# Kernel tuning notes

Hardware: AMD Instinct MI355X
Metric: run time of the kernel (lower is better)

## Reference

```python
import jax, jax.numpy as jnp
import numpy as np

N_NODES = 50000
N_EDGES = 800000
IN_DIM = 128
HID = 32
HEADS = 4
OUT_DIM = 128
NEG_SLOPE = 0.2


def setup_inputs() -> dict:
    key = jax.random.key(0)
    ks = jax.random.split(key, 10)
    s = lambda fan_in: 1.0 / np.sqrt(fan_in)
    return {
        "x": jax.random.normal(ks[0], (N_NODES, IN_DIM), dtype=jnp.float32),
        "edge_index": jax.random.randint(ks[1], (2, N_EDGES), 0, N_NODES, dtype=jnp.int64),
        # encoder GATConv: in=IN_DIM, out=HID, heads=HEADS (concat)
        "W1": jax.random.normal(ks[2], (IN_DIM, HEADS * HID), dtype=jnp.float32) * s(IN_DIM),
        "att_src1": jax.random.normal(ks[3], (HEADS, HID), dtype=jnp.float32) * s(HID),
        "att_dst1": jax.random.normal(ks[4], (HEADS, HID), dtype=jnp.float32) * s(HID),
        "b1": jnp.zeros((HEADS * HID,), dtype=jnp.float32),
        # decoder GATConv: in=HEADS*HID, out=OUT_DIM, heads=1
        "W2": jax.random.normal(ks[5], (HEADS * HID, OUT_DIM), dtype=jnp.float32) * s(HEADS * HID),
        "att_src2": jax.random.normal(ks[6], (1, OUT_DIM), dtype=jnp.float32) * s(OUT_DIM),
        "att_dst2": jax.random.normal(ks[7], (1, OUT_DIM), dtype=jnp.float32) * s(OUT_DIM),
        "b2": jnp.zeros((OUT_DIM,), dtype=jnp.float32),
    }


def _gat_conv(x, src, dst, W, att_src, att_dst, bias, heads, out_ch):
    """PyG-style GATConv (v1), eval mode (dropout off), self-loops already in src/dst."""
    n = x.shape[0]
    h = (x @ W).reshape(n, heads, out_ch)                 # [N,H,C]
    a_src = jnp.einsum("nhc,hc->nh", h, att_src)          # [N,H]
    a_dst = jnp.einsum("nhc,hc->nh", h, att_dst)          # [N,H]
    e = jax.nn.leaky_relu(a_src[src] + a_dst[dst], NEG_SLOPE)  # [E,H]
    # segment softmax over destination neighborhoods
    e_max = jax.ops.segment_max(e, dst, num_segments=n)   # [N,H]
    e_exp = jnp.exp(e - e_max[dst])
    denom = jax.ops.segment_sum(e_exp, dst, num_segments=n)
    alpha = e_exp / (denom[dst] + 1e-16)                  # [E,H]
    msg = h[src] * alpha[:, :, None]                      # [E,H,C]
    out = jax.ops.segment_sum(msg, dst, num_segments=n)   # [N,H,C]
    return out.reshape(n, heads * out_ch) + bias


def reference(x, edge_index, W1, att_src1, att_dst1, b1, W2, att_src2, att_dst2, b2):
    n = x.shape[0]
    loops = jnp.arange(n, dtype=edge_index.dtype)
    src = jnp.concatenate([edge_index[0], loops])
    dst = jnp.concatenate([edge_index[1], loops])
    z = jax.nn.relu(_gat_conv(x, src, dst, W1, att_src1, att_dst1, b1, HEADS, HID))
    x_hat = jax.nn.relu(_gat_conv(z, src, dst, W2, att_src2, att_dst2, b2, 1, OUT_DIM))
    return x_hat
```

## Files before the change

### kernel.cpp

```cpp
#include <hip/hip_runtime.h>
#include <hip/hip_bf16.h>
#include <cstddef>

#define N_NODES 50000
#define N_EDGES_RAW 800000
#define E_TOT (N_EDGES_RAW + N_NODES)
#define DIM 128
#define NEG_SLOPE 0.2f

#define NBUCK 196
#define CHUNK 4096
#define NBLK_E ((E_TOT + CHUNK - 1) / CHUNK)
#define CONV_BLKS 3125
#define GB 782

typedef __attribute__((ext_vector_type(8))) short bf16x8;
typedef __attribute__((ext_vector_type(4))) float f32x4;

__device__ __forceinline__ ushort f2bf(float f) {
  unsigned u = __float_as_uint(f);
  return (ushort)((u + 0x7FFFu + ((u >> 16) & 1u)) >> 16);
}
__device__ __forceinline__ float bf2f_lo(uint u) {
  return __uint_as_float(u << 16);
}
__device__ __forceinline__ float bf2f_hi(uint u) {
  return __uint_as_float(u & 0xFFFF0000u);
}

__device__ __forceinline__ void get_edge(const int* __restrict__ ei, int is64,
                                         int e, int& s, int& d) {
  if (e >= N_EDGES_RAW) { s = e - N_EDGES_RAW; d = s; return; }
  if (is64) {
    s = ei[2 * (size_t)e];
    d = ei[2 * ((size_t)N_EDGES_RAW + (size_t)e)];
  } else {
    s = ei[e];
    d = ei[N_EDGES_RAW + e];
  }
}

__device__ __forceinline__ int detect_inline(const int* __restrict__ ei,
                                             int* sflag) {
  const int t = threadIdx.x;
  if (t < 64) {
    int hi = ei[2 * t + 1];
    unsigned long long b = __ballot(hi != 0);
    if (t == 0) *sflag = (b == 0ULL) ? 1 : 0;
  }
  __syncthreads();
  return *sflag;
}

__device__ __forceinline__ void prep_one(const float* __restrict__ w,
                                         const float* __restrict__ atts,
                                         const float* __restrict__ attd,
                                         ushort* __restrict__ wtx,
                                         int H, int idx) {
  const int c = idx >> 7, k = idx & 127;
  const int C = 128 / H;
  float v;
  if (c < 128) {
    v = w[k * 128 + c];
  } else if (c < 128 + H) {
    const int hd = c - 128;
    float s = 0.f;
    for (int j = 0; j < C; ++j) s += w[k * 128 + hd * C + j] * atts[hd * C + j];
    v = s;
  } else if (c < 128 + 2 * H) {
    const int hd = c - 128 - H;
    float s = 0.f;
    for (int j = 0; j < C; ++j) s += w[k * 128 + hd * C + j] * attd[hd * C + j];
    v = s;
  } else {
    v = 0.f;
  }
  wtx[idx] = f2bf(v);
}

__global__ __launch_bounds__(256) void mega_setup(
    const float* __restrict__ W1, const float* __restrict__ as1,
    const float* __restrict__ ad1, ushort* __restrict__ wtx1,
    const float* __restrict__ W2, const float* __restrict__ as2,
    const float* __restrict__ ad2, ushort* __restrict__ wtx2,
    const float* __restrict__ x, ushort* __restrict__ x_bf,
    const int* __restrict__ ei, int* __restrict__ hist_mat,
    unsigned* __restrict__ pairs) {
  const int b = blockIdx.x, t = threadIdx.x;
  if (b < 72) {
    prep_one(W1, as1, ad1, wtx1, 4, b * 256 + t);
  } else if (b < 144) {
    prep_one(W2, as2, ad2, wtx2, 1, (b - 72) * 256 + t);
  } else if (b < 144 + CONV_BLKS) {
    const int base = (b - 144) * 2048 + t * 8;
    float4 v0 = *(const float4*)(x + base);
    float4 v1 = *(const float4*)(x + base + 4);
    ushort u[8];
    u[0] = f2bf(v0.x); u[1] = f2bf(v0.y); u[2] = f2bf(v0.z); u[3] = f2bf(v0.w);
    u[4] = f2bf(v1.x); u[5] = f2bf(v1.y); u[6] = f2bf(v1.z); u[7] = f2bf(v1.w);
    *(uint4*)(x_bf + base) = *(const uint4*)u;
  } else {
    __shared__ int hist[NBUCK];
    __shared__ int sflag;
    const int cb = b - 144 - CONV_BLKS;
    if (t < NBUCK) hist[t] = 0;
    const int is64 = detect_inline(ei, &sflag);
    __syncthreads();
    const int e0 = cb * CHUNK;
#pragma unroll
    for (int i = 0; i < CHUNK / 256; ++i) {
      int e = e0 + i * 256 + t;
      if (e < E_TOT) {
        int s, d;
        get_edge(ei, is64, e, s, d);
        pairs[e] = (unsigned)s | ((unsigned)d << 16);
        atomicAdd(&hist[d >> 8], 1);
      }
    }
    __syncthreads();
    if (t < NBUCK) hist_mat[cb * NBUCK + t] = hist[t];
  }
}

__global__ __launch_bounds__(256) void bucket_scatter(
    const unsigned* __restrict__ pairs, const int* __restrict__ hist_mat,
    unsigned* __restrict__ tmp, int* __restrict__ bstart_g) {
  __shared__ int wtot[4];
  __shared__ int sbase[NBUCK];
  __shared__ int shist[NBUCK];
  const int b = blockIdx.x, t = threadIdx.x, lane = t & 63, wid = t >> 6;
  int tot = 0, pre = 0;
  if (t < NBUCK) {
    for (int bb = 0; bb < NBLK_E; ++bb) {
      int v = hist_mat[bb * NBUCK + t];
      pre += (bb < b) ? v : 0;
      tot += v;
    }
    shist[t] = 0;
  }
  int sc = tot;
#pragma unroll
  for (int m = 1; m < 64; m <<= 1) {
    int o = __shfl_up(sc, m, 64);
    if (lane >= m) sc += o;
  }
  if (lane == 63) wtot[wid] = sc;
  __syncthreads();
  int off = 0;
  for (int w = 0; w < wid; ++w) off += wtot[w];
  const int excl = off + sc - tot;
  if (t < NBUCK) sbase[t] = excl + pre;
  if (b == 0) {
    if (t < NBUCK) bstart_g[t] = excl;
    if (t == 255) bstart_g[NBUCK] = off + sc;
  }
  __syncthreads();
  const int e0 = b * CHUNK;
  unsigned pr_[CHUNK / 256];
  int rk[CHUNK / 256];
#pragma unroll
  for (int i = 0; i < CHUNK / 256; ++i) {
    int e = e0 + i * 256 + t;
    if (e < E_TOT) {
      unsigned pr = pairs[e];
      pr_[i] = pr;
      rk[i] = atomicAdd(&shist[pr >> 24], 1);
    }
  }
#pragma unroll
  for (int i = 0; i < CHUNK / 256; ++i) {
    int e = e0 + i * 256 + t;
    if (e < E_TOT) tmp[sbase[pr_[i] >> 24] + rk[i]] = pr_[i];
  }
}

__device__ __forceinline__ void bucket_sort_body(int b,
                                                 const unsigned* __restrict__ tmp,
                                                 const int* __restrict__ bstart,
                                                 int* __restrict__ csr_src,
                                                 int* __restrict__ rp,
                                                 int* __restrict__ deg) {
  __shared__ int cnt[256];
  __shared__ int cur[256];
  __shared__ int wtot2[4];
  const int t = threadIdx.x, lane = t & 63, wid = t >> 6;
  const int p0 = bstart[b], p1 = bstart[b + 1];
  cnt[t] = 0;
  __syncthreads();
  for (int j = p0 + t; j < p1; j += 256) {
    unsigned pr = tmp[j];
    atomicAdd(&cnt[(pr >> 16) & 255u], 1);
  }
  __syncthreads();
  int v = cnt[t];
  int sc = v;
#pragma unroll
  for (int m = 1; m < 64; m <<= 1) {
    int o = __shfl_up(sc, m, 64);
    if (lane >= m) sc += o;
  }
  if (lane == 63) wtot2[wid] = sc;
  __syncthreads();
  int off = 0;
  for (int w = 0; w < wid; ++w) off += wtot2[w];
  const int excl = off + sc - v;
  const int node = b * 256 + t;
  if (node < N_NODES) {
    deg[node] = v;
    rp[node] = p0 + excl;
  }
  cur[t] = excl;
  __syncthreads();
  for (int j = p0 + t; j < p1; j += 256) {
    unsigned pr = tmp[j];
    int ld = (int)((pr >> 16) & 255u);
    int r = atomicAdd(&cur[ld], 1);
    csr_src[p0 + r] = (int)(pr & 0xFFFFu);
  }
}

template <int H>
__device__ __forceinline__ void gemm_att_body(int blk,
                                              const ushort* __restrict__ in_bf,
                                              const ushort* __restrict__ wtx,
                                              ushort* __restrict__ h_bf,
                                              float* __restrict__ a_src,
                                              float* __restrict__ a_dst) {
  const int wid = threadIdx.x >> 6;
  const int lane = threadIdx.x & 63;
  const int tile = blk * 4 + wid;
  if (tile >= N_NODES / 16) return;
  const int row0 = tile * 16;
  const int rA = lane & 15;
  const int g = lane >> 4;

  f32x4 acc[9];
#pragma unroll
  for (int ct = 0; ct < 9; ++ct) acc[ct] = (f32x4){0.f, 0.f, 0.f, 0.f};

#pragma unroll
  for (int ks = 0; ks < 4; ++ks) {
    const int k0 = ks * 32 + g * 8;
    bf16x8 af = *(const bf16x8*)(in_bf + (size_t)(row0 + rA) * DIM + k0);
#pragma unroll
    for (int ct = 0; ct < 9; ++ct) {
      bf16x8 bf = *(const bf16x8*)(wtx + (size_t)(ct * 16 + rA) * 128 + k0);
      acc[ct] = __builtin_amdgcn_mfma_f32_16x16x32_bf16(af, bf, acc[ct], 0, 0, 0);
    }
  }

#pragma unroll
  for (int ct = 0; ct < 8; ++ct) {
#pragma unroll
    for (int r = 0; r < 4; ++r) {
      const int row = row0 + g * 4 + r;
      h_bf[(size_t)row * DIM + ct * 16 + rA] = f2bf(acc[ct][r]);
    }
  }
  if (rA < 2 * H) {
#pragma unroll
    for (int r = 0; r < 4; ++r) {
      const int row = row0 + g * 4 + r;
      if (rA < H)
        a_src[(size_t)row * H + rA] = acc[8][r];
      else
        a_dst[(size_t)row * H + (rA - H)] = acc[8][r];
    }
  }
}

__global__ __launch_bounds__(256) void gemm4_sort(
    const ushort* __restrict__ x_bf, const ushort* __restrict__ wtx1,
    ushort* __restrict__ h_bf, float* __restrict__ a_src,
    float* __restrict__ a_dst, const unsigned* __restrict__ tmp,
    const int* __restrict__ bstart, int* __restrict__ csr_src,
    int* __restrict__ rp, int* __restrict__ deg) {
  if (blockIdx.x < GB)
    gemm_att_body<4>(blockIdx.x, x_bf, wtx1, h_bf, a_src, a_dst);
  else
    bucket_sort_body(blockIdx.x - GB, tmp, bstart, csr_src, rp, deg);
}

__global__ __launch_bounds__(256) void gemm_att1(const ushort* __restrict__ in_bf,
                                                 const ushort* __restrict__ wtx,
                                                 ushort* __restrict__ h_bf,
                                                 float* __restrict__ a_src,
                                                 float* __restrict__ a_dst) {
  gemm_att_body<1>(blockIdx.x, in_bf, wtx, h_bf, a_src, a_dst);
}

template <int H, bool OBF>
__global__ __launch_bounds__(256) void node_agg(const int* __restrict__ rp,
                                                const int* __restrict__ deg,
                                                const int* __restrict__ csr_src,
                                                const ushort* __restrict__ h_bf,
                                                const float* __restrict__ a_src,
                                                const float* __restrict__ a_dst,
                                                const float* __restrict__ bias,
                                                void* __restrict__ outp) {
  __shared__ float p_lds[4][H][64];
  __shared__ int s_lds[4][64];
  const int wid = threadIdx.x >> 6;
  const int lane = threadIdx.x & 63;
  const int node = blockIdx.x * 4 + wid;
  if (node >= N_NODES) return;
  const int head = (H == 4) ? (lane >> 4) : 0;
  const int beg = rp[node];
  const int dg = deg[node];
  const int* __restrict__ srcs = csr_src + beg;

  float ad[H];
#pragma unroll
  for (int h = 0; h < H; ++h) ad[h] = a_dst[(size_t)node * H + h];

  float sden[H];
#pragma unroll
  for (int h = 0; h < H; ++h) sden[h] = 0.f;
  float ax = 0.f, ay = 0.f;

  for (int c0 = 0; c0 < dg; c0 += 64) {
    const int cnt = min(64, dg - c0);
    if (lane < cnt) {
      int s = srcs[c0 + lane];
      s_lds[wid][lane] = s;
      if (H == 4) {
        float4 as4 = ((const float4*)a_src)[s];
        float vv[4] = {as4.x, as4.y, as4.z, as4.w};
#pragma unroll
        for (int h = 0; h < 4; ++h) {
          float v = vv[h] + ad[h];
          v = v > 0.f ? v : NEG_SLOPE * v;
          v = fminf(fmaxf(v, -60.f), 80.f);
          float p = __expf(v);
          sden[h] += p;
          p_lds[wid][h][lane] = p;
        }
      } else {
        float v = a_src[s] + ad[0];
        v = v > 0.f ? v : NEG_SLOPE * v;
        v = fminf(fmaxf(v, -60.f), 80.f);
        float p = __expf(v);
        sden[0] += p;
        p_lds[wid][0][lane] = p;
      }
    }
    int j = 0;
    for (; j + 8 <= cnt; j += 8) {
#pragma unroll
      for (int u = 0; u < 8; ++u) {
        int s = s_lds[wid][j + u];
        float p = p_lds[wid][head][j + u];
        uint hv = *(const uint*)(h_bf + (size_t)s * DIM + 2 * lane);
        ax += p * bf2f_lo(hv);
        ay += p * bf2f_hi(hv);
      }
    }
    for (; j < cnt; ++j) {
      int s = s_lds[wid][j];
      float p = p_lds[wid][head][j];
      uint hv = *(const uint*)(h_bf + (size_t)s * DIM + 2 * lane);
      ax += p * bf2f_lo(hv);
      ay += p * bf2f_hi(hv);
    }
  }

#pragma unroll
  for (int h = 0; h < H; ++h) {
#pragma unroll
    for (int m = 1; m < 64; m <<= 1) sden[h] += __shfl_xor(sden[h], m);
  }
  const float inv = 1.f / sden[head];

  float2 bv = ((const float2*)bias)[lane];
  float ox = fmaxf(ax * inv + bv.x, 0.f);
  float oy = fmaxf(ay * inv + bv.y, 0.f);
  if (OBF) {
    uint u = (uint)f2bf(ox) | ((uint)f2bf(oy) << 16);
    ((uint*)((ushort*)outp + (size_t)node * DIM))[lane] = u;
  } else {
    ((float2*)((float*)outp + (size_t)node * DIM))[lane] = make_float2(ox, oy);
  }
}

extern "C" void kernel_launch(void* const* d_in, const int* in_sizes, int n_in,
                              void* d_out, int out_size, void* d_ws, size_t ws_size,
                              hipStream_t stream) {
  const float* x   = (const float*)d_in[0];
  const int*   ei  = (const int*)d_in[1];
  const float* W1  = (const float*)d_in[2];
  const float* as1 = (const float*)d_in[3];
  const float* ad1 = (const float*)d_in[4];
  const float* b1  = (const float*)d_in[5];
  const float* W2  = (const float*)d_in[6];
  const float* as2 = (const float*)d_in[7];
  const float* ad2 = (const float*)d_in[8];
  const float* b2  = (const float*)d_in[9];
  float* out = (float*)d_out;

  char* ws = (char*)d_ws;
  const size_t F_H = (size_t)N_NODES * DIM;
  ushort*   h_bf    = (ushort*)ws;
  ushort*   z_bf    = h_bf + F_H;
  ushort*   x_bf    = z_bf + F_H;
  float*    a_src   = (float*)(x_bf + F_H);
  float*    a_dst   = a_src + 200000;
  int*      deg     = (int*)(a_dst + 200000);
  int*      rp      = deg + N_NODES;
  int*      csr_src = rp + N_NODES;
  unsigned* tmp     = (unsigned*)(csr_src + E_TOT);
  unsigned* pairs   = tmp + E_TOT;
  int*      hist_mat= (int*)(pairs + E_TOT);
  int*      bstart  = hist_mat + NBLK_E * NBUCK;
  ushort*   wtx1    = (ushort*)(bstart + NBUCK + 3);
  ushort*   wtx2    = wtx1 + 144 * 128;

  const int MEGA = 144 + CONV_BLKS + NBLK_E;

  hipLaunchKernelGGL(mega_setup, dim3(MEGA), dim3(256), 0, stream,
                     W1, as1, ad1, wtx1, W2, as2, ad2, wtx2, x, x_bf, ei,
                     hist_mat, pairs);
  hipLaunchKernelGGL(bucket_scatter, dim3(NBLK_E), dim3(256), 0, stream,
                     pairs, hist_mat, tmp, bstart);
  hipLaunchKernelGGL(gemm4_sort, dim3(GB + NBUCK), dim3(256), 0, stream,
                     x_bf, wtx1, h_bf, a_src, a_dst, tmp, bstart, csr_src, rp, deg);
  hipLaunchKernelGGL((node_agg<4, true>), dim3((N_NODES + 3) / 4), dim3(256), 0,
                     stream, rp, deg, csr_src, h_bf, a_src, a_dst, b1, z_bf);

  hipLaunchKernelGGL(gemm_att1, dim3(GB), dim3(256), 0, stream,
                     z_bf, wtx2, h_bf, a_src, a_dst);
  hipLaunchKernelGGL((node_agg<1, false>), dim3((N_NODES + 3) / 4), dim3(256), 0,
                     stream, rp, deg, csr_src, h_bf, a_src, a_dst, b2, out);
}
```

Before: 165.6 us.

## Aggregate 16 nodes per block with block-cooperative edge score precompute

Each node-aggregation block now covers 16 consecutive nodes, and each wave handles 4 of them in turn. The block's contiguous CSR edge range is staged in 512-edge chunks, and all 256 threads compute the exp scores into LDS together, instead of each wave working only on its own node's few edges. To make this possible, the CSR array now stores the packed (dst, src) word, so the dst attention term can be looked up per edge. The softmax denominator is accumulated per lane in the gather loop, which removes the cross-lane shuffle reductions. The cost is block-level barriers, a quarter as many blocks, and serial per-node gathers within each wave.

```diff
diff --git a/kernel.cpp b/kernel.cpp
--- a/kernel.cpp
+++ b/kernel.cpp
@@ -13,6 +13,7 @@
 #define NBLK_E ((E_TOT + CHUNK - 1) / CHUNK)
 #define CONV_BLKS 3125
 #define GB 782
+#define ECHUNK 512
 
 typedef __attribute__((ext_vector_type(8))) short bf16x8;
 typedef __attribute__((ext_vector_type(4))) float f32x4;
@@ -177,7 +178,7 @@
 __device__ __forceinline__ void bucket_sort_body(int b,
                                                  const unsigned* __restrict__ tmp,
                                                  const int* __restrict__ bstart,
-                                                 int* __restrict__ csr_src,
+                                                 unsigned* __restrict__ csr2,
                                                  int* __restrict__ rp,
                                                  int* __restrict__ deg) {
   __shared__ int cnt[256];
@@ -215,7 +216,7 @@
     unsigned pr = tmp[j];
     int ld = (int)((pr >> 16) & 255u);
     int r = atomicAdd(&cur[ld], 1);
-    csr_src[p0 + r] = (int)(pr & 0xFFFFu);
+    csr2[p0 + r] = pr;
   }
 }
 
@@ -273,12 +274,12 @@
     const ushort* __restrict__ x_bf, const ushort* __restrict__ wtx1,
     ushort* __restrict__ h_bf, float* __restrict__ a_src,
     float* __restrict__ a_dst, const unsigned* __restrict__ tmp,
-    const int* __restrict__ bstart, int* __restrict__ csr_src,
+    const int* __restrict__ bstart, unsigned* __restrict__ csr2,
     int* __restrict__ rp, int* __restrict__ deg) {
   if (blockIdx.x < GB)
     gemm_att_body<4>(blockIdx.x, x_bf, wtx1, h_bf, a_src, a_dst);
   else
-    bucket_sort_body(blockIdx.x - GB, tmp, bstart, csr_src, rp, deg);
+    bucket_sort_body(blockIdx.x - GB, tmp, bstart, csr2, rp, deg);
 }
 
 __global__ __launch_bounds__(256) void gemm_att1(const ushort* __restrict__ in_bf,
@@ -292,93 +293,90 @@
 template <int H, bool OBF>
 __global__ __launch_bounds__(256) void node_agg(const int* __restrict__ rp,
                                                 const int* __restrict__ deg,
-                                                const int* __restrict__ csr_src,
+                                                const unsigned* __restrict__ csr2,
                                                 const ushort* __restrict__ h_bf,
                                                 const float* __restrict__ a_src,
                                                 const float* __restrict__ a_dst,
                                                 const float* __restrict__ bias,
                                                 void* __restrict__ outp) {
-  __shared__ float p_lds[4][H][64];
-  __shared__ int s_lds[4][64];
-  const int wid = threadIdx.x >> 6;
-  const int lane = threadIdx.x & 63;
-  const int node = blockIdx.x * 4 + wid;
-  if (node >= N_NODES) return;
+  __shared__ float p_lds[ECHUNK][H];
+  __shared__ int s_lds[ECHUNK];
+  const int t = threadIdx.x;
+  const int wid = t >> 6;
+  const int lane = t & 63;
+  const int nbase = blockIdx.x * 16;
   const int head = (H == 4) ? (lane >> 4) : 0;
-  const int beg = rp[node];
-  const int dg = deg[node];
-  const int* __restrict__ srcs = csr_src + beg;
-
-  float ad[H];
-#pragma unroll
-  for (int h = 0; h < H; ++h) ad[h] = a_dst[(size_t)node * H + h];
-
-  float sden[H];
-#pragma unroll
-  for (int h = 0; h < H; ++h) sden[h] = 0.f;
-  float ax = 0.f, ay = 0.f;
-
-  for (int c0 = 0; c0 < dg; c0 += 64) {
-    const int cnt = min(64, dg - c0);
-    if (lane < cnt) {
-      int s = srcs[c0 + lane];
-      s_lds[wid][lane] = s;
+
+  int rp_m[4], dg_m[4];
+#pragma unroll
+  for (int m = 0; m < 4; ++m) {
+    int n = nbase + 4 * wid + m;
+    rp_m[m] = rp[n];
+    dg_m[m] = deg[n];
+  }
+  const int blockbase = rp[nbase];
+  const int blockend = rp[nbase + 15] + deg[nbase + 15];
+
+  float ax[4], ay[4], sden[4];
+#pragma unroll
+  for (int m = 0; m < 4; ++m) { ax[m] = 0.f; ay[m] = 0.f; sden[m] = 0.f; }
+
+  for (int base = blockbase; base < blockend; base += ECHUNK) {
+    const int cnt = min(ECHUNK, blockend - base);
+    for (int k = t; k < cnt; k += 256) {
+      unsigned pr = csr2[base + k];
+      int s = (int)(pr & 0xFFFFu);
+      int d = (int)(pr >> 16);
+      s_lds[k] = s;
       if (H == 4) {
         float4 as4 = ((const float4*)a_src)[s];
-        float vv[4] = {as4.x, as4.y, as4.z, as4.w};
+        float4 ad4 = ((const float4*)a_dst)[d];
+        float vv[4] = {as4.x + ad4.x, as4.y + ad4.y, as4.z + ad4.z, as4.w + ad4.w};
 #pragma unroll
         for (int h = 0; h < 4; ++h) {
-          float v = vv[h] + ad[h];
+          float v = vv[h];
           v = v > 0.f ? v : NEG_SLOPE * v;
           v = fminf(fmaxf(v, -60.f), 80.f);
-          float p = __expf(v);
-          sden[h] += p;
-          p_lds[wid][h][lane] = p;
+          p_lds[k][h] = __expf(v);
         }
       } else {
-        float v = a_src[s] + ad[0];
+        float v = a_src[s] + a_dst[d];
         v = v > 0.f ? v : NEG_SLOPE * v;
         v = fminf(fmaxf(v, -60.f), 80.f);
-        float p = __expf(v);
-        sden[0] += p;
-        p_lds[wid][0][lane] = p;
+        p_lds[k][0] = __expf(v);
       }
     }
-    int j = 0;
-    for (; j + 8 <= cnt; j += 8) {
-#pragma unroll
-      for (int u = 0; u < 8; ++u) {
-        int s = s_lds[wid][j + u];
-        float p = p_lds[wid][head][j + u];
+    __syncthreads();
+#pragma unroll
+    for (int m = 0; m < 4; ++m) {
+      const int lo = max(rp_m[m], base) - base;
+      const int hi = min(rp_m[m] + dg_m[m], base + cnt) - base;
+#pragma unroll 2
+      for (int j = lo; j < hi; ++j) {
+        int s = s_lds[j];
+        float p = p_lds[j][head];
         uint hv = *(const uint*)(h_bf + (size_t)s * DIM + 2 * lane);
-        ax += p * bf2f_lo(hv);
-        ay += p * bf2f_hi(hv);
+        ax[m] += p * bf2f_lo(hv);
+        ay[m] += p * bf2f_hi(hv);
+        sden[m] += p;
       }
     }
-    for (; j < cnt; ++j) {
-      int s = s_lds[wid][j];
-      float p = p_lds[wid][head][j];
-      uint hv = *(const uint*)(h_bf + (size_t)s * DIM + 2 * lane);
-      ax += p * bf2f_lo(hv);
-      ay += p * bf2f_hi(hv);
-    }
-  }
-
-#pragma unroll
-  for (int h = 0; h < H; ++h) {
-#pragma unroll
-    for (int m = 1; m < 64; m <<= 1) sden[h] += __shfl_xor(sden[h], m);
-  }
-  const float inv = 1.f / sden[head];
-
-  float2 bv = ((const float2*)bias)[lane];
-  float ox = fmaxf(ax * inv + bv.x, 0.f);
-  float oy = fmaxf(ay * inv + bv.y, 0.f);
-  if (OBF) {
-    uint u = (uint)f2bf(ox) | ((uint)f2bf(oy) << 16);
-    ((uint*)((ushort*)outp + (size_t)node * DIM))[lane] = u;
-  } else {
-    ((float2*)((float*)outp + (size_t)node * DIM))[lane] = make_float2(ox, oy);
+    __syncthreads();
+  }
+
+  const float2 bv = ((const float2*)bias)[lane];
+#pragma unroll
+  for (int m = 0; m < 4; ++m) {
+    const int node = nbase + 4 * wid + m;
+    const float inv = 1.f / sden[m];
+    float ox = fmaxf(ax[m] * inv + bv.x, 0.f);
+    float oy = fmaxf(ay[m] * inv + bv.y, 0.f);
+    if (OBF) {
+      uint u = (uint)f2bf(ox) | ((uint)f2bf(oy) << 16);
+      ((uint*)((ushort*)outp + (size_t)node * DIM))[lane] = u;
+    } else {
+      ((float2*)((float*)outp + (size_t)node * DIM))[lane] = make_float2(ox, oy);
+    }
   }
 }
 
@@ -406,8 +404,8 @@
   float*    a_dst   = a_src + 200000;
   int*      deg     = (int*)(a_dst + 200000);
   int*      rp      = deg + N_NODES;
-  int*      csr_src = rp + N_NODES;
-  unsigned* tmp     = (unsigned*)(csr_src + E_TOT);
+  unsigned* csr2    = (unsigned*)(rp + N_NODES);
+  unsigned* tmp     = csr2 + E_TOT;
   unsigned* pairs   = tmp + E_TOT;
   int*      hist_mat= (int*)(pairs + E_TOT);
   int*      bstart  = hist_mat + NBLK_E * NBUCK;
@@ -415,6 +413,7 @@
   ushort*   wtx2    = wtx1 + 144 * 128;
 
   const int MEGA = 144 + CONV_BLKS + NBLK_E;
+  const int AGG_B = N_NODES / 16;
 
   hipLaunchKernelGGL(mega_setup, dim3(MEGA), dim3(256), 0, stream,
                      W1, as1, ad1, wtx1, W2, as2, ad2, wtx2, x, x_bf, ei,
@@ -422,12 +421,12 @@
   hipLaunchKernelGGL(bucket_scatter, dim3(NBLK_E), dim3(256), 0, stream,
                      pairs, hist_mat, tmp, bstart);
   hipLaunchKernelGGL(gemm4_sort, dim3(GB + NBUCK), dim3(256), 0, stream,
-                     x_bf, wtx1, h_bf, a_src, a_dst, tmp, bstart, csr_src, rp, deg);
-  hipLaunchKernelGGL((node_agg<4, true>), dim3((N_NODES + 3) / 4), dim3(256), 0,
-                     stream, rp, deg, csr_src, h_bf, a_src, a_dst, b1, z_bf);
+                     x_bf, wtx1, h_bf, a_src, a_dst, tmp, bstart, csr2, rp, deg);
+  hipLaunchKernelGGL((node_agg<4, true>), dim3(AGG_B), dim3(256), 0, stream,
+                     rp, deg, csr2, h_bf, a_src, a_dst, b1, z_bf);
 
   hipLaunchKernelGGL(gemm_att1, dim3(GB), dim3(256), 0, stream,
                      z_bf, wtx2, h_bf, a_src, a_dst);
-  hipLaunchKernelGGL((node_agg<1, false>), dim3((N_NODES + 3) / 4), dim3(256), 0,
-                     stream, rp, deg, csr_src, h_bf, a_src, a_dst, b2, out);
-}
+  hipLaunchKernelGGL((node_agg<1, false>), dim3(AGG_B), dim3(256), 0, stream,
+                     rp, deg, csr2, h_bf, a_src, a_dst, b2, out);
+}
```

After: 176.6 us. 6.6% more time.
